# Optimization experiments

Hardware: AMD Instinct MI355X
Metric: run time of the kernel (lower is better)

The kernel has to match this reference:

```python
import jax, jax.numpy as jnp
import numpy as np

PATCH = 7
PAD = PATCH // 2  # 3


def _to_gray(x):
    # x: [B,3,H,W] -> [B,1,H,W]
    return 0.299 * x[:, 0:1] + 0.587 * x[:, 1:2] + 0.114 * x[:, 2:3]


def _census_transform(x):
    # x: [B,C,H,W] RGB -> grayscale, then 48 shifted binary comparisons.
    if x.shape[1] == 3:
        x = _to_gray(x)
    B, C, H, W = x.shape
    x_pad = jnp.pad(x, ((0, 0), (0, 0), (PAD, PAD), (PAD, PAD)), mode='reflect')
    center = x
    feats = []
    for i in range(PATCH):
        for j in range(PATCH):
            if i == PAD and j == PAD:
                continue
            neighbor = x_pad[:, :, i:i + H, j:j + W]
            feats.append((center > neighbor).astype(x.dtype))
    return jnp.concatenate(feats, axis=1)  # [B,48,H,W]


def setup_inputs() -> dict:
    key = jax.random.key(0)
    k1, k2 = jax.random.split(key)
    B, C, H, W = 8, 3, 512, 512
    pred = jax.random.uniform(k1, (B, C, H, W), dtype=jnp.float32)
    target = jax.random.uniform(k2, (B, C, H, W), dtype=jnp.float32)
    return {"pred": pred, "target": target}


def reference(pred, target):
    pred_census = _census_transform(pred)
    target_census = _census_transform(target)
    return jnp.abs(pred_census - target_census).mean()
```

## Files before the change

### kernel.cpp

```cpp
#include <hip/hip_runtime.h>


#define BATCH 8
#define HH 512
#define WW 512
#define PLANE (HH * WW)
#define TW 64
#define TH 64
#define SCOLS 72
#define HROWS 70
#define S1 38
#define S2 (HROWS - S1)
#define KPR 18
#define PITCH 76
#define NT 512

__device__ __forceinline__ int refl(int v, int n) {
    return v < 0 ? -v : (v >= n ? 2 * n - 2 - v : v);
}

__device__ __forceinline__ void load_col(const float* col, float (&w)[14]) {
    const float4 a = *(const float4*)(col);
    const float4 b = *(const float4*)(col + 4);
    const float4 c = *(const float4*)(col + 8);
    const float2 d = *(const float2*)(col + 12);
    w[0] = a.x;  w[1] = a.y;  w[2]  = a.z; w[3]  = a.w;
    w[4] = b.x;  w[5] = b.y;  w[6]  = b.z; w[7]  = b.w;
    w[8] = c.x;  w[9] = c.y;  w[10] = c.z; w[11] = c.w;
    w[12] = d.x; w[13] = d.y;
}

__global__ __launch_bounds__(NT, 4)
void census_fused(const float* __restrict__ pred,
                  const float* __restrict__ target,
                  float* __restrict__ out) {
    __shared__ __align__(16) float sP[SCOLS][PITCH];
    __shared__ __align__(16) float sT[SCOLS][PITCH];

    const int b   = blockIdx.z;
    const int ty0 = blockIdx.y * TH;
    const int tx0 = blockIdx.x * TW;
    const float* __restrict__ pb = pred   + (size_t)b * 3 * PLANE;
    const float* __restrict__ tb = target + (size_t)b * 3 * PLANE;
    const bool fastx = (blockIdx.x >= 1 && blockIdx.x <= 6);

    auto stage_fast = [&](int hy, int k) {
        const int gy  = refl(ty0 + hy - 3, HH);
        const int off = gy * WW + tx0 - 4 + 4 * k;
        const float4 pr = *(const float4*)(pb + off);
        const float4 pg = *(const float4*)(pb + off + PLANE);
        const float4 pc = *(const float4*)(pb + off + 2 * PLANE);
        const float4 tr = *(const float4*)(tb + off);
        const float4 tg = *(const float4*)(tb + off + PLANE);
        const float4 tc = *(const float4*)(tb + off + 2 * PLANE);
        const int lx = 4 * k;
        sP[lx + 0][hy] = 0.299f * pr.x + 0.587f * pg.x + 0.114f * pc.x;
        sP[lx + 1][hy] = 0.299f * pr.y + 0.587f * pg.y + 0.114f * pc.y;
        sP[lx + 2][hy] = 0.299f * pr.z + 0.587f * pg.z + 0.114f * pc.z;
        sP[lx + 3][hy] = 0.299f * pr.w + 0.587f * pg.w + 0.114f * pc.w;
        sT[lx + 0][hy] = 0.299f * tr.x + 0.587f * tg.x + 0.114f * tc.x;
        sT[lx + 1][hy] = 0.299f * tr.y + 0.587f * tg.y + 0.114f * tc.y;
        sT[lx + 2][hy] = 0.299f * tr.z + 0.587f * tg.z + 0.114f * tc.z;
        sT[lx + 3][hy] = 0.299f * tr.w + 0.587f * tg.w + 0.114f * tc.w;
    };
    auto stage_scalar = [&](int hy, int lx) {
        const int gy  = refl(ty0 + hy - 3, HH);
        const int gx  = refl(tx0 + lx - 4, WW);
        const int off = gy * WW + gx;
        sP[lx][hy] = 0.299f * pb[off] + 0.587f * pb[off + PLANE] + 0.114f * pb[off + 2 * PLANE];
        sT[lx][hy] = 0.299f * tb[off] + 0.587f * tb[off + PLANE] + 0.114f * tb[off + 2 * PLANE];
    };

    if (fastx) {
        for (int idx = threadIdx.x; idx < S1 * KPR; idx += NT) {
            const int hy = idx / KPR;
            stage_fast(hy, idx - hy * KPR);
        }
    } else {
        for (int idx = threadIdx.x; idx < S1 * SCOLS; idx += NT) {
            const int hy = idx / SCOLS;
            stage_scalar(hy, idx - hy * SCOLS);
        }
    }
    __syncthreads();

    const int wv = threadIdx.x >> 6;
    const int c  = threadIdx.x & 63;

    auto band_count = [&](int pr0) -> int {
        float wP[14], wT[14], cP[8], cT[8];
        int cnt = 0;
        load_col(&sP[c + 4][pr0], wP);
        load_col(&sT[c + 4][pr0], wT);
        #pragma unroll
        for (int p = 0; p < 8; ++p) { cP[p] = wP[3 + p]; cT[p] = wT[3 + p]; }
        #pragma unroll
        for (int p = 0; p < 8; ++p) {
            #pragma unroll
            for (int dy = -3; dy <= 3; ++dy) {
                if (dy == 0) continue;
                cnt += ((cP[p] > wP[3 + p + dy]) != (cT[p] > wT[3 + p + dy])) ? 1 : 0;
            }
        }
        #pragma unroll
        for (int t = 0; t < 6; ++t) {
            const int lx = c + 1 + (t < 3 ? t : t + 1);
            load_col(&sP[lx][pr0], wP);
            load_col(&sT[lx][pr0], wT);
            #pragma unroll
            for (int p = 0; p < 8; ++p) {
                #pragma unroll
                for (int dy = -3; dy <= 3; ++dy)
                    cnt += ((cP[p] > wP[3 + p + dy]) != (cT[p] > wT[3 + p + dy])) ? 1 : 0;
            }
        }
        return cnt;
    };

    int cnt = 0;
    if (wv < 4) {
        cnt = band_count(wv * 8);
    } else {
        const int t2 = threadIdx.x - 256;
        if (fastx) {
            for (int idx = t2; idx < S2 * KPR; idx += 256) {
                const int r = idx / KPR;
                stage_fast(S1 + r, idx - r * KPR);
            }
        } else {
            for (int idx = t2; idx < S2 * SCOLS; idx += 256) {
                const int r = idx / SCOLS;
                stage_scalar(S1 + r, idx - r * SCOLS);
            }
        }
    }
    __syncthreads();
    if (wv >= 4) cnt = band_count(wv * 8);

    #pragma unroll
    for (int o = 32; o > 0; o >>= 1) cnt += __shfl_down(cnt, o, 64);
    __shared__ int wsum[8];
    if ((threadIdx.x & 63) == 0) wsum[wv] = cnt;
    __syncthreads();
    if (threadIdx.x == 0) {
        int tot = 0;
        #pragma unroll
        for (int w = 0; w < 8; ++w) tot += wsum[w];
        atomicAdd(out, (float)tot * (1.0f / 100663296.0f));
    }
}

extern "C" void kernel_launch(void* const* d_in, const int* in_sizes, int n_in,
                              void* d_out, int out_size, void* d_ws, size_t ws_size,
                              hipStream_t stream) {
    const float* pred   = (const float*)d_in[0];
    const float* target = (const float*)d_in[1];
    float* out = (float*)d_out;

    hipMemsetAsync(out, 0, sizeof(float), stream);

    dim3 grid(WW / TW, HH / TH, BATCH);
    census_fused<<<grid, NT, 0, stream>>>(pred, target, out);
}
```

Before: 114.4 us.

## Halve tile height, swizzle LDS columns, raise occupancy to 8 blocks

Tile height drops from 64 to 32 rows, so each thread handles 4 pixels instead of 8 and LDS per block shrinks. An XOR-like per-column offset (cbase) skews the column-major LDS layout to reduce bank conflicts on the vector column loads. Launch bounds rise to 8 blocks per CU to improve latency hiding. In exchange, the vertical halo overhead grows (38 staged rows per 32 output rows instead of 70 per 64), the grid doubles, and the number of atomics doubles.

```diff
diff --git a/kernel.cpp b/kernel.cpp
--- a/kernel.cpp
+++ b/kernel.cpp
@@ -6,36 +6,38 @@
 #define WW 512
 #define PLANE (HH * WW)
 #define TW 64
-#define TH 64
+#define TH 32
 #define SCOLS 72
-#define HROWS 70
-#define S1 38
+#define HROWS 38
+#define S1 22
 #define S2 (HROWS - S1)
 #define KPR 18
-#define PITCH 76
+#define PITCH 44
 #define NT 512
+#define LDSZ (SCOLS * PITCH)
 
 __device__ __forceinline__ int refl(int v, int n) {
     return v < 0 ? -v : (v >= n ? 2 * n - 2 - v : v);
 }
+__device__ __forceinline__ int cbase(int lx) {
+    return lx * PITCH + (((lx >> 2) & 7) << 2);
+}
 
-__device__ __forceinline__ void load_col(const float* col, float (&w)[14]) {
+__device__ __forceinline__ void load_col10(const float* col, float (&w)[10]) {
     const float4 a = *(const float4*)(col);
     const float4 b = *(const float4*)(col + 4);
-    const float4 c = *(const float4*)(col + 8);
-    const float2 d = *(const float2*)(col + 12);
-    w[0] = a.x;  w[1] = a.y;  w[2]  = a.z; w[3]  = a.w;
-    w[4] = b.x;  w[5] = b.y;  w[6]  = b.z; w[7]  = b.w;
-    w[8] = c.x;  w[9] = c.y;  w[10] = c.z; w[11] = c.w;
-    w[12] = d.x; w[13] = d.y;
+    const float2 d = *(const float2*)(col + 8);
+    w[0] = a.x; w[1] = a.y; w[2] = a.z; w[3] = a.w;
+    w[4] = b.x; w[5] = b.y; w[6] = b.z; w[7] = b.w;
+    w[8] = d.x; w[9] = d.y;
 }
 
-__global__ __launch_bounds__(NT, 4)
+__global__ __launch_bounds__(NT, 8)
 void census_fused(const float* __restrict__ pred,
                   const float* __restrict__ target,
                   float* __restrict__ out) {
-    __shared__ __align__(16) float sP[SCOLS][PITCH];
-    __shared__ __align__(16) float sT[SCOLS][PITCH];
+    __shared__ __align__(16) float sP[LDSZ];
+    __shared__ __align__(16) float sT[LDSZ];
 
     const int b   = blockIdx.z;
     const int ty0 = blockIdx.y * TH;
@@ -54,21 +56,21 @@
         const float4 tg = *(const float4*)(tb + off + PLANE);
         const float4 tc = *(const float4*)(tb + off + 2 * PLANE);
         const int lx = 4 * k;
-        sP[lx + 0][hy] = 0.299f * pr.x + 0.587f * pg.x + 0.114f * pc.x;
-        sP[lx + 1][hy] = 0.299f * pr.y + 0.587f * pg.y + 0.114f * pc.y;
-        sP[lx + 2][hy] = 0.299f * pr.z + 0.587f * pg.z + 0.114f * pc.z;
-        sP[lx + 3][hy] = 0.299f * pr.w + 0.587f * pg.w + 0.114f * pc.w;
-        sT[lx + 0][hy] = 0.299f * tr.x + 0.587f * tg.x + 0.114f * tc.x;
-        sT[lx + 1][hy] = 0.299f * tr.y + 0.587f * tg.y + 0.114f * tc.y;
-        sT[lx + 2][hy] = 0.299f * tr.z + 0.587f * tg.z + 0.114f * tc.z;
-        sT[lx + 3][hy] = 0.299f * tr.w + 0.587f * tg.w + 0.114f * tc.w;
+        sP[cbase(lx + 0) + hy] = 0.299f * pr.x + 0.587f * pg.x + 0.114f * pc.x;
+        sP[cbase(lx + 1) + hy] = 0.299f * pr.y + 0.587f * pg.y + 0.114f * pc.y;
+        sP[cbase(lx + 2) + hy] = 0.299f * pr.z + 0.587f * pg.z + 0.114f * pc.z;
+        sP[cbase(lx + 3) + hy] = 0.299f * pr.w + 0.587f * pg.w + 0.114f * pc.w;
+        sT[cbase(lx + 0) + hy] = 0.299f * tr.x + 0.587f * tg.x + 0.114f * tc.x;
+        sT[cbase(lx + 1) + hy] = 0.299f * tr.y + 0.587f * tg.y + 0.114f * tc.y;
+        sT[cbase(lx + 2) + hy] = 0.299f * tr.z + 0.587f * tg.z + 0.114f * tc.z;
+        sT[cbase(lx + 3) + hy] = 0.299f * tr.w + 0.587f * tg.w + 0.114f * tc.w;
     };
     auto stage_scalar = [&](int hy, int lx) {
         const int gy  = refl(ty0 + hy - 3, HH);
         const int gx  = refl(tx0 + lx - 4, WW);
         const int off = gy * WW + gx;
-        sP[lx][hy] = 0.299f * pb[off] + 0.587f * pb[off + PLANE] + 0.114f * pb[off + 2 * PLANE];
-        sT[lx][hy] = 0.299f * tb[off] + 0.587f * tb[off + PLANE] + 0.114f * tb[off + 2 * PLANE];
+        sP[cbase(lx) + hy] = 0.299f * pb[off] + 0.587f * pb[off + PLANE] + 0.114f * pb[off + 2 * PLANE];
+        sT[cbase(lx) + hy] = 0.299f * tb[off] + 0.587f * tb[off + PLANE] + 0.114f * tb[off + 2 * PLANE];
     };
 
     if (fastx) {
@@ -88,14 +90,14 @@
     const int c  = threadIdx.x & 63;
 
     auto band_count = [&](int pr0) -> int {
-        float wP[14], wT[14], cP[8], cT[8];
+        float wP[10], wT[10], cP[4], cT[4];
         int cnt = 0;
-        load_col(&sP[c + 4][pr0], wP);
-        load_col(&sT[c + 4][pr0], wT);
+        load_col10(&sP[cbase(c + 4) + pr0], wP);
+        load_col10(&sT[cbase(c + 4) + pr0], wT);
         #pragma unroll
-        for (int p = 0; p < 8; ++p) { cP[p] = wP[3 + p]; cT[p] = wT[3 + p]; }
+        for (int p = 0; p < 4; ++p) { cP[p] = wP[3 + p]; cT[p] = wT[3 + p]; }
         #pragma unroll
-        for (int p = 0; p < 8; ++p) {
+        for (int p = 0; p < 4; ++p) {
             #pragma unroll
             for (int dy = -3; dy <= 3; ++dy) {
                 if (dy == 0) continue;
@@ -105,10 +107,10 @@
         #pragma unroll
         for (int t = 0; t < 6; ++t) {
             const int lx = c + 1 + (t < 3 ? t : t + 1);
-            load_col(&sP[lx][pr0], wP);
-            load_col(&sT[lx][pr0], wT);
+            load_col10(&sP[cbase(lx) + pr0], wP);
+            load_col10(&sT[cbase(lx) + pr0], wT);
             #pragma unroll
-            for (int p = 0; p < 8; ++p) {
+            for (int p = 0; p < 4; ++p) {
                 #pragma unroll
                 for (int dy = -3; dy <= 3; ++dy)
                     cnt += ((cP[p] > wP[3 + p + dy]) != (cT[p] > wT[3 + p + dy])) ? 1 : 0;
@@ -119,7 +121,7 @@
 
     int cnt = 0;
     if (wv < 4) {
-        cnt = band_count(wv * 8);
+        cnt = band_count(wv * 4);
     } else {
         const int t2 = threadIdx.x - 256;
         if (fastx) {
@@ -135,7 +137,7 @@
         }
     }
     __syncthreads();
-    if (wv >= 4) cnt = band_count(wv * 8);
+    if (wv >= 4) cnt = band_count(wv * 4);
 
     #pragma unroll
     for (int o = 32; o > 0; o >>= 1) cnt += __shfl_down(cnt, o, 64);
```

New measurement: 123.5 us. 1.08x slower.
